# Optimization experiments

Measured on AMD Instinct MI355X. Metric: run time of the kernel, lower is better.

Reference implementation:

```python
import jax, jax.numpy as jnp
import numpy as np

N_NODES = 100000
N_EDGES = 1600000
D_IN = 128
HID = 256
N_CLASSES = 10
N_GRAPHS = 512


def setup_inputs() -> dict:
    key = jax.random.key(0)
    ks = jax.random.split(key, 12)
    x = jax.random.normal(ks[0], (N_NODES, D_IN), dtype=jnp.float32)
    edge_index = jax.random.randint(ks[1], (2, N_EDGES), 0, N_NODES, dtype=jnp.int32)
    batch = jnp.sort(jax.random.randint(ks[2], (N_NODES,), 0, N_GRAPHS, dtype=jnp.int32))
    s = 0.05
    return {
        "x": x,
        "edge_index": edge_index,
        "batch": batch,
        "W1": jax.random.normal(ks[3], (D_IN, HID), dtype=jnp.float32) * s,
        "b1": jnp.zeros((HID,), dtype=jnp.float32),
        "W2": jax.random.normal(ks[4], (HID, HID), dtype=jnp.float32) * s,
        "b2": jnp.zeros((HID,), dtype=jnp.float32),
        "fc1_w": jax.random.normal(ks[5], (HID, HID // 2), dtype=jnp.float32) * s,
        "fc1_b": jnp.zeros((HID // 2,), dtype=jnp.float32),
        "fc2_w": jax.random.normal(ks[6], (HID // 2, N_CLASSES), dtype=jnp.float32) * s,
        "fc2_b": jnp.zeros((N_CLASSES,), dtype=jnp.float32),
    }


def gcn_conv(x, src, dst, W, b, num_nodes):
    # PyG GCNConv: h = x @ W, add self-loops, sym-normalized scatter-add, + bias
    h = x @ W  # [N, out]
    loop = jnp.arange(num_nodes, dtype=src.dtype)
    s = jnp.concatenate([src, loop])
    d = jnp.concatenate([dst, loop])
    ones = jnp.ones(s.shape[0], dtype=h.dtype)
    deg = jax.ops.segment_sum(ones, d, num_segments=num_nodes)  # includes self-loops
    dinv = jax.lax.rsqrt(jnp.maximum(deg, 1.0))
    norm = dinv[s] * dinv[d]  # [E+N]
    msgs = h[s] * norm[:, None]  # gather + scale
    out = jax.ops.segment_sum(msgs, d, num_segments=num_nodes)  # scatter-add
    return out + b


def global_mean_pool(x, batch, num_graphs):
    sums = jax.ops.segment_sum(x, batch, num_segments=num_graphs)
    cnt = jax.ops.segment_sum(jnp.ones(x.shape[0], x.dtype), batch, num_segments=num_graphs)
    return sums / jnp.maximum(cnt, 1.0)[:, None]


def reference(x, edge_index, batch, W1, b1, W2, b2, fc1_w, fc1_b, fc2_w, fc2_b):
    src, dst = edge_index[0], edge_index[1]
    h = jax.nn.relu(gcn_conv(x, src, dst, W1, b1, N_NODES))
    h = jax.nn.relu(gcn_conv(h, src, dst, W2, b2, N_NODES))
    g = global_mean_pool(h, batch, N_GRAPHS)  # [G, HID]
    # dropout is identity in eval mode
    g = jax.nn.relu(g @ fc1_w + fc1_b)
    return g @ fc2_w + fc2_b  # [G, num_classes]
```

## Files before the change

kernel.cpp:

```cpp
#include <hip/hip_runtime.h>
#include <hip/hip_bf16.h>
#include <hip/hip_fp16.h>
#include <cstddef>

#define N_NODES 100000
#define N_EDGES 1600000
#define D_IN 128
#define HID 256
#define N_CLASSES 10
#define N_GRAPHS 512
#define CAP 64

typedef __attribute__((ext_vector_type(8))) short short8v;
typedef __attribute__((ext_vector_type(4))) float f32x4;
typedef _Float16 h2v __attribute__((ext_vector_type(2)));
typedef _Float16 h4v __attribute__((ext_vector_type(4)));
typedef _Float16 h8v __attribute__((ext_vector_type(8)));

__device__ __forceinline__ ushort f2bf(float x) {
    __hip_bfloat16 b = __float2bfloat16(x);
    return *reinterpret_cast<ushort*>(&b);
}
__device__ __forceinline__ float bf2f(ushort u) {
    __hip_bfloat16 b = *reinterpret_cast<__hip_bfloat16*>(&u);
    return __bfloat162float(b);
}

__global__ void zero_int_kernel(int* p, int n) {
    int i = blockIdx.x * blockDim.x + threadIdx.x;
    if (i < n) p[i] = 0;
}

__global__ void fill_bins_kernel(const int* __restrict__ src, const int* __restrict__ dst,
                                 int* __restrict__ cnt, int* __restrict__ bins) {
    int t = blockIdx.x * blockDim.x + threadIdx.x;
    int base = t * 4;
    if (base + 4 <= N_EDGES) {
        int4 d4 = *reinterpret_cast<const int4*>(dst + base);
        int4 s4 = *reinterpret_cast<const int4*>(src + base);
        int k0 = atomicAdd(&cnt[d4.x], 1);
        int k1 = atomicAdd(&cnt[d4.y], 1);
        int k2 = atomicAdd(&cnt[d4.z], 1);
        int k3 = atomicAdd(&cnt[d4.w], 1);
        if (k0 < CAP) __builtin_nontemporal_store(s4.x, &bins[(size_t)d4.x * CAP + k0]);
        if (k1 < CAP) __builtin_nontemporal_store(s4.y, &bins[(size_t)d4.y * CAP + k1]);
        if (k2 < CAP) __builtin_nontemporal_store(s4.z, &bins[(size_t)d4.z * CAP + k2]);
        if (k3 < CAP) __builtin_nontemporal_store(s4.w, &bins[(size_t)d4.w * CAP + k3]);
    } else {
        for (int e = base; e < N_EDGES; ++e) {
            int d = dst[e];
            int k = atomicAdd(&cnt[d], 1);
            if (k < CAP) __builtin_nontemporal_store(src[e], &bins[(size_t)d * CAP + k]);
        }
    }
}

__global__ void dinv_kernel(const int* __restrict__ cnt, float* __restrict__ dinv, int n) {
    int i = blockIdx.x * blockDim.x + threadIdx.x;
    if (i < n) dinv[i] = rsqrtf((float)(1 + cnt[i]));
}

__global__ void wsplit_kernel(const float* __restrict__ W, ushort* __restrict__ Wh,
                              ushort* __restrict__ Wl, int K, int M) {
    int idx = blockIdx.x * blockDim.x + threadIdx.x;
    if (idx >= M * K) return;
    int m = idx / K, k = idx - m * K;
    float v = W[(size_t)k * M + m];
    ushort h = f2bf(v);
    Wh[idx] = h;
    Wl[idx] = f2bf(v - bf2f(h));
}

__global__ void xscale_kernel(const float* __restrict__ x, const float* __restrict__ dinv,
                              _Float16* __restrict__ xh) {
    int idx = blockIdx.x * blockDim.x + threadIdx.x;
    if (idx >= N_NODES * D_IN / 8) return;
    int node = idx >> 4;
    float s = dinv[node];
    const float4 a = *reinterpret_cast<const float4*>(x + (size_t)idx * 8);
    const float4 b = *reinterpret_cast<const float4*>(x + (size_t)idx * 8 + 4);
    h8v o;
    o[0] = (_Float16)(a.x * s); o[1] = (_Float16)(a.y * s);
    o[2] = (_Float16)(a.z * s); o[3] = (_Float16)(a.w * s);
    o[4] = (_Float16)(b.x * s); o[5] = (_Float16)(b.y * s);
    o[6] = (_Float16)(b.z * s); o[7] = (_Float16)(b.w * s);
    *reinterpret_cast<h8v*>(xh + (size_t)idx * 8) = o;
}

#define GPAD 40
__global__ __launch_bounds__(256) void gemm_bf16x2_kernel(
    const ushort* __restrict__ Ah, const ushort* __restrict__ Al,
    const ushort* __restrict__ Bh, const ushort* __restrict__ Bl,
    _Float16* __restrict__ C, const float* __restrict__ bias,
    const float* __restrict__ rowscale, int N, int K, int M) {
    __shared__ ushort AhL[128 * GPAD];
    __shared__ ushort AlL[128 * GPAD];
    __shared__ ushort BhL[128 * GPAD];
    __shared__ ushort BlL[128 * GPAD];

    int tid = threadIdx.x;
    int lane = tid & 63, w = tid >> 6;
    int wr = w >> 1, wc = w & 1;
    int rowBase = blockIdx.y * 128;
    int colBase = blockIdx.x * 128;

    f32x4 acc[4][4];
#pragma unroll
    for (int m = 0; m < 4; ++m)
#pragma unroll
        for (int n = 0; n < 4; ++n) acc[m][n] = (f32x4)(0.0f);

    const uint4 zero4 = make_uint4(0, 0, 0, 0);

    for (int k0 = 0; k0 < K; k0 += 32) {
#pragma unroll
        for (int c = 0; c < 2; ++c) {
            int idx = c * 256 + tid;
            int r = idx >> 2, q = idx & 3;
            int lds = r * GPAD + q * 8;
            size_t ga = (size_t)(rowBase + r) * K + k0 + q * 8;
            uint4 va = zero4, vl = zero4;
            if (rowBase + r < N) {
                va = *reinterpret_cast<const uint4*>(Ah + ga);
                vl = *reinterpret_cast<const uint4*>(Al + ga);
            }
            *reinterpret_cast<uint4*>(&AhL[lds]) = va;
            *reinterpret_cast<uint4*>(&AlL[lds]) = vl;
            size_t gb = (size_t)(colBase + r) * K + k0 + q * 8;
            *reinterpret_cast<uint4*>(&BhL[lds]) = *reinterpret_cast<const uint4*>(Bh + gb);
            *reinterpret_cast<uint4*>(&BlL[lds]) = *reinterpret_cast<const uint4*>(Bl + gb);
        }
        __syncthreads();

        short8v afh[4], afl[4], bfh[4], bfl[4];
        int kg = (lane >> 4) * 8;
#pragma unroll
        for (int m = 0; m < 4; ++m) {
            int r = wr * 64 + m * 16 + (lane & 15);
            afh[m] = *reinterpret_cast<const short8v*>(&AhL[r * GPAD + kg]);
            afl[m] = *reinterpret_cast<const short8v*>(&AlL[r * GPAD + kg]);
        }
#pragma unroll
        for (int n = 0; n < 4; ++n) {
            int r = wc * 64 + n * 16 + (lane & 15);
            bfh[n] = *reinterpret_cast<const short8v*>(&BhL[r * GPAD + kg]);
            bfl[n] = *reinterpret_cast<const short8v*>(&BlL[r * GPAD + kg]);
        }
#pragma unroll
        for (int m = 0; m < 4; ++m)
#pragma unroll
            for (int n = 0; n < 4; ++n) {
                acc[m][n] = __builtin_amdgcn_mfma_f32_16x16x32_bf16(afh[m], bfh[n], acc[m][n], 0, 0, 0);
                acc[m][n] = __builtin_amdgcn_mfma_f32_16x16x32_bf16(afh[m], bfl[n], acc[m][n], 0, 0, 0);
                acc[m][n] = __builtin_amdgcn_mfma_f32_16x16x32_bf16(afl[m], bfh[n], acc[m][n], 0, 0, 0);
            }
        __syncthreads();
    }

    float bv[4];
#pragma unroll
    for (int n = 0; n < 4; ++n)
        bv[n] = bias[colBase + wc * 64 + n * 16 + (lane & 15)];

#pragma unroll
    for (int m = 0; m < 4; ++m) {
#pragma unroll
        for (int reg = 0; reg < 4; ++reg) {
            int row = rowBase + wr * 64 + m * 16 + (lane >> 4) * 4 + reg;
            if (row < N) {
                float sc = rowscale ? rowscale[row] : 1.0f;
#pragma unroll
                for (int n = 0; n < 4; ++n) {
                    int col = colBase + wc * 64 + n * 16 + (lane & 15);
                    C[(size_t)row * M + col] = (_Float16)(fmaxf(acc[m][n][reg] + bv[n], 0.0f) * sc);
                }
            }
        }
    }
}

__global__ __launch_bounds__(256) void gather_h_kernel(
    const _Float16* __restrict__ hf, const int* __restrict__ bins,
    const int* __restrict__ cnt, const float* __restrict__ dinv,
    ushort* __restrict__ aggH, ushort* __restrict__ aggL) {
    int node = blockIdx.x * 4 + (threadIdx.x >> 6);
    if (node >= N_NODES) return;
    int lane = threadIdx.x & 63;
    const size_t dimOff = (size_t)lane * 4;
    const size_t binBase = (size_t)node * CAP;

    h4v hv = *reinterpret_cast<const h4v*>(hf + (size_t)node * HID + dimOff);
    float4 a[4];
    a[0] = make_float4((float)hv[0], (float)hv[1], (float)hv[2], (float)hv[3]);
    a[1] = make_float4(0.f, 0.f, 0.f, 0.f);
    a[2] = make_float4(0.f, 0.f, 0.f, 0.f);
    a[3] = make_float4(0.f, 0.f, 0.f, 0.f);

    int end = min(cnt[node], CAP);
    int e = 0;
    for (; e + 12 <= end; e += 12) {
        int ss[12];
#pragma unroll
        for (int k = 0; k < 12; ++k) ss[k] = bins[binBase + e + k];
        h4v vv[12];
#pragma unroll
        for (int k = 0; k < 12; ++k)
            vv[k] = *reinterpret_cast<const h4v*>(hf + (size_t)ss[k] * HID + dimOff);
#pragma unroll
        for (int k = 0; k < 12; ++k) {
            a[k & 3].x += (float)vv[k][0];
            a[k & 3].y += (float)vv[k][1];
            a[k & 3].z += (float)vv[k][2];
            a[k & 3].w += (float)vv[k][3];
        }
    }
    for (; e < end; ++e) {
        int s = bins[binBase + e];
        h4v v = *reinterpret_cast<const h4v*>(hf + (size_t)s * HID + dimOff);
        a[0].x += (float)v[0]; a[0].y += (float)v[1];
        a[0].z += (float)v[2]; a[0].w += (float)v[3];
    }
    float dn = dinv[node];
    float4 acc = make_float4(((a[0].x + a[1].x) + (a[2].x + a[3].x)) * dn,
                             ((a[0].y + a[1].y) + (a[2].y + a[3].y)) * dn,
                             ((a[0].z + a[1].z) + (a[2].z + a[3].z)) * dn,
                             ((a[0].w + a[1].w) + (a[2].w + a[3].w)) * dn);
    ushort4 hh, ll;
    hh.x = f2bf(acc.x); ll.x = f2bf(acc.x - bf2f(hh.x));
    hh.y = f2bf(acc.y); ll.y = f2bf(acc.y - bf2f(hh.y));
    hh.z = f2bf(acc.z); ll.z = f2bf(acc.z - bf2f(hh.z));
    hh.w = f2bf(acc.w); ll.w = f2bf(acc.w - bf2f(hh.w));
    *reinterpret_cast<ushort4*>(aggH + (size_t)node * HID + dimOff) = hh;
    *reinterpret_cast<ushort4*>(aggL + (size_t)node * HID + dimOff) = ll;
}

__global__ __launch_bounds__(256) void gather_x_kernel(
    const _Float16* __restrict__ xh, const int* __restrict__ bins,
    const int* __restrict__ cnt, const float* __restrict__ dinv,
    ushort* __restrict__ aggH, ushort* __restrict__ aggL) {
    int node = blockIdx.x * 4 + (threadIdx.x >> 6);
    if (node >= N_NODES) return;
    int lane = threadIdx.x & 63;
    const size_t dimOff = (size_t)lane * 2;
    const size_t binBase = (size_t)node * CAP;

    h2v hv = *reinterpret_cast<const h2v*>(xh + (size_t)node * D_IN + dimOff);
    float2 a[4];
    a[0] = make_float2((float)hv[0], (float)hv[1]);
    a[1] = make_float2(0.f, 0.f);
    a[2] = make_float2(0.f, 0.f);
    a[3] = make_float2(0.f, 0.f);

    int end = min(cnt[node], CAP);
    int e = 0;
    for (; e + 12 <= end; e += 12) {
        int ss[12];
#pragma unroll
        for (int k = 0; k < 12; ++k) ss[k] = bins[binBase + e + k];
        h2v vv[12];
#pragma unroll
        for (int k = 0; k < 12; ++k)
            vv[k] = *reinterpret_cast<const h2v*>(xh + (size_t)ss[k] * D_IN + dimOff);
#pragma unroll
        for (int k = 0; k < 12; ++k) {
            a[k & 3].x += (float)vv[k][0];
            a[k & 3].y += (float)vv[k][1];
        }
    }
    for (; e < end; ++e) {
        int s = bins[binBase + e];
        h2v v = *reinterpret_cast<const h2v*>(xh + (size_t)s * D_IN + dimOff);
        a[0].x += (float)v[0]; a[0].y += (float)v[1];
    }
    float dn = dinv[node];
    float2 acc = make_float2(((a[0].x + a[1].x) + (a[2].x + a[3].x)) * dn,
                             ((a[0].y + a[1].y) + (a[2].y + a[3].y)) * dn);
    ushort2 hh, ll;
    hh.x = f2bf(acc.x); ll.x = f2bf(acc.x - bf2f(hh.x));
    hh.y = f2bf(acc.y); ll.y = f2bf(acc.y - bf2f(hh.y));
    *reinterpret_cast<ushort2*>(aggH + (size_t)node * D_IN + dimOff) = hh;
    *reinterpret_cast<ushort2*>(aggL + (size_t)node * D_IN + dimOff) = ll;
}

__global__ __launch_bounds__(256) void pool_head_kernel(
    const _Float16* __restrict__ h, const int* __restrict__ batch,
    const float* __restrict__ fc1_w, const float* __restrict__ fc1_b,
    const float* __restrict__ fc2_w, const float* __restrict__ fc2_b,
    float* __restrict__ out) {
    __shared__ int sRange[2];
    __shared__ float gbuf[HID];
    __shared__ float hbuf[HID / 2];
    int g = blockIdx.x;
    int tid = threadIdx.x;

    if (tid < 2) {
        int target = g + tid;
        int lo = 0, hi = N_NODES;
        while (lo < hi) {
            int mid = (lo + hi) >> 1;
            if (batch[mid] < target) lo = mid + 1; else hi = mid;
        }
        sRange[tid] = lo;
    }
    __syncthreads();
    int beg = sRange[0], end = sRange[1];

    float acc = 0.f;
    int n = beg;
    for (; n + 4 <= end; n += 4) {
        float v0 = (float)h[(size_t)(n + 0) * HID + tid];
        float v1 = (float)h[(size_t)(n + 1) * HID + tid];
        float v2 = (float)h[(size_t)(n + 2) * HID + tid];
        float v3 = (float)h[(size_t)(n + 3) * HID + tid];
        acc += (v0 + v1) + (v2 + v3);
    }
    for (; n < end; ++n) acc += (float)h[(size_t)n * HID + tid];
    float c = fmaxf((float)(end - beg), 1.0f);
    gbuf[tid] = acc / c;
    __syncthreads();

    if (tid < HID / 2) {
        float a = fc1_b[tid];
        for (int k = 0; k < HID; ++k) a += gbuf[k] * fc1_w[(size_t)k * (HID / 2) + tid];
        hbuf[tid] = fmaxf(a, 0.0f);
    }
    __syncthreads();
    if (tid < N_CLASSES) {
        float a = fc2_b[tid];
        for (int k = 0; k < HID / 2; ++k) a += hbuf[k] * fc2_w[(size_t)k * N_CLASSES + tid];
        out[(size_t)g * N_CLASSES + tid] = a;
    }
}

extern "C" void kernel_launch(void* const* d_in, const int* in_sizes, int n_in,
                              void* d_out, int out_size, void* d_ws, size_t ws_size,
                              hipStream_t stream) {
    const float* x     = (const float*)d_in[0];
    const int* eidx    = (const int*)d_in[1];
    const int* batch   = (const int*)d_in[2];
    const float* W1    = (const float*)d_in[3];
    const float* b1    = (const float*)d_in[4];
    const float* W2    = (const float*)d_in[5];
    const float* b2    = (const float*)d_in[6];
    const float* fc1_w = (const float*)d_in[7];
    const float* fc1_b = (const float*)d_in[8];
    const float* fc2_w = (const float*)d_in[9];
    const float* fc2_b = (const float*)d_in[10];
    float* out = (float*)d_out;

    const int* src = eidx;
    const int* dst = eidx + N_EDGES;

    _Float16* h16  = (_Float16*)d_ws;
    _Float16* xh   = h16;
    ushort* R2     = (ushort*)(h16 + (size_t)N_NODES * HID);
    ushort* aggXh  = R2;
    ushort* aggXl  = R2 + (size_t)N_NODES * D_IN;
    ushort* aggHh  = R2;
    ushort* aggHl  = R2 + (size_t)N_NODES * HID;
    int* bins      = (int*)(R2 + (size_t)2 * N_NODES * HID);
    ushort* Wt1h   = (ushort*)(bins + (size_t)N_NODES * CAP);
    ushort* Wt1l   = Wt1h + HID * D_IN;
    ushort* Wt2h   = Wt1l + HID * D_IN;
    ushort* Wt2l   = Wt2h + HID * HID;
    float* dinv    = (float*)(Wt2l + HID * HID);
    int* cnt       = (int*)(dinv + N_NODES);

    const int nB = (N_NODES + 255) / 256;

    zero_int_kernel<<<nB, 256, 0, stream>>>(cnt, N_NODES);
    fill_bins_kernel<<<(N_EDGES / 4 + 255) / 256, 256, 0, stream>>>(src, dst, cnt, bins);
    dinv_kernel<<<nB, 256, 0, stream>>>(cnt, dinv, N_NODES);

    wsplit_kernel<<<(HID * D_IN + 255) / 256, 256, 0, stream>>>(W1, Wt1h, Wt1l, D_IN, HID);
    wsplit_kernel<<<(HID * HID + 255) / 256, 256, 0, stream>>>(W2, Wt2h, Wt2l, HID, HID);
    xscale_kernel<<<(N_NODES * D_IN / 8 + 255) / 256, 256, 0, stream>>>(x, dinv, xh);

    const int gatherBlocks = (N_NODES + 3) / 4;
    dim3 gemmGrid(HID / 128, (N_NODES + 127) / 128);

    gather_x_kernel<<<gatherBlocks, 256, 0, stream>>>(xh, bins, cnt, dinv, aggXh, aggXl);
    gemm_bf16x2_kernel<<<gemmGrid, 256, 0, stream>>>(aggXh, aggXl, Wt1h, Wt1l, h16, b1, dinv,
                                                     N_NODES, D_IN, HID);

    gather_h_kernel<<<gatherBlocks, 256, 0, stream>>>(h16, bins, cnt, dinv, aggHh, aggHl);
    gemm_bf16x2_kernel<<<gemmGrid, 256, 0, stream>>>(aggHh, aggHl, Wt2h, Wt2l, h16, b2, nullptr,
                                                     N_NODES, HID, HID);

    pool_head_kernel<<<N_GRAPHS, 256, 0, stream>>>(h16, batch, fc1_w, fc1_b, fc2_w, fc2_b, out);
}
```

Before: 621.0 us.

## Load neighbor bins once per wave and broadcast indices via shuffles

In both gather kernels each lane now loads one bin entry in a single coalesced read, and neighbor indices are broadcast with __shfl, replacing the scalar-uniform loads from the bins array. The unroll depth drops from 12 to 8. fill_bins goes back to one edge per thread with plain stores instead of vectorized int4 loads and nontemporal stores, and the zero kernel becomes hipMemsetAsync. The shuffles add cross-lane ops, the smaller unroll lowers memory-level parallelism, and the simpler fill kernel may change the cost of the scatter.

New measurement: 549.0 us. -11.6%, faster.

```diff
diff --git a/kernel.cpp b/kernel.cpp
--- a/kernel.cpp
+++ b/kernel.cpp
@@ -26,32 +26,13 @@
     return __bfloat162float(b);
 }
 
-__global__ void zero_int_kernel(int* p, int n) {
-    int i = blockIdx.x * blockDim.x + threadIdx.x;
-    if (i < n) p[i] = 0;
-}
-
 __global__ void fill_bins_kernel(const int* __restrict__ src, const int* __restrict__ dst,
-                                 int* __restrict__ cnt, int* __restrict__ bins) {
-    int t = blockIdx.x * blockDim.x + threadIdx.x;
-    int base = t * 4;
-    if (base + 4 <= N_EDGES) {
-        int4 d4 = *reinterpret_cast<const int4*>(dst + base);
-        int4 s4 = *reinterpret_cast<const int4*>(src + base);
-        int k0 = atomicAdd(&cnt[d4.x], 1);
-        int k1 = atomicAdd(&cnt[d4.y], 1);
-        int k2 = atomicAdd(&cnt[d4.z], 1);
-        int k3 = atomicAdd(&cnt[d4.w], 1);
-        if (k0 < CAP) __builtin_nontemporal_store(s4.x, &bins[(size_t)d4.x * CAP + k0]);
-        if (k1 < CAP) __builtin_nontemporal_store(s4.y, &bins[(size_t)d4.y * CAP + k1]);
-        if (k2 < CAP) __builtin_nontemporal_store(s4.z, &bins[(size_t)d4.z * CAP + k2]);
-        if (k3 < CAP) __builtin_nontemporal_store(s4.w, &bins[(size_t)d4.w * CAP + k3]);
-    } else {
-        for (int e = base; e < N_EDGES; ++e) {
-            int d = dst[e];
-            int k = atomicAdd(&cnt[d], 1);
-            if (k < CAP) __builtin_nontemporal_store(src[e], &bins[(size_t)d * CAP + k]);
-        }
+                                 int* __restrict__ cnt, int* __restrict__ bins, int nE) {
+    int e = blockIdx.x * blockDim.x + threadIdx.x;
+    if (e < nE) {
+        int d = dst[e];
+        int k = atomicAdd(&cnt[d], 1);
+        if (k < CAP) bins[(size_t)d * CAP + k] = src[e];
     }
 }
 
@@ -187,7 +168,9 @@
     if (node >= N_NODES) return;
     int lane = threadIdx.x & 63;
     const size_t dimOff = (size_t)lane * 4;
-    const size_t binBase = (size_t)node * CAP;
+
+    int myBin = bins[(size_t)node * CAP + lane];
+    int end = min(cnt[node], CAP);
 
     h4v hv = *reinterpret_cast<const h4v*>(hf + (size_t)node * HID + dimOff);
     float4 a[4];
@@ -196,18 +179,17 @@
     a[2] = make_float4(0.f, 0.f, 0.f, 0.f);
     a[3] = make_float4(0.f, 0.f, 0.f, 0.f);
 
-    int end = min(cnt[node], CAP);
     int e = 0;
-    for (; e + 12 <= end; e += 12) {
-        int ss[12];
-#pragma unroll
-        for (int k = 0; k < 12; ++k) ss[k] = bins[binBase + e + k];
-        h4v vv[12];
-#pragma unroll
-        for (int k = 0; k < 12; ++k)
+    for (; e + 8 <= end; e += 8) {
+        int ss[8];
+#pragma unroll
+        for (int k = 0; k < 8; ++k) ss[k] = __shfl(myBin, e + k);
+        h4v vv[8];
+#pragma unroll
+        for (int k = 0; k < 8; ++k)
             vv[k] = *reinterpret_cast<const h4v*>(hf + (size_t)ss[k] * HID + dimOff);
 #pragma unroll
-        for (int k = 0; k < 12; ++k) {
+        for (int k = 0; k < 8; ++k) {
             a[k & 3].x += (float)vv[k][0];
             a[k & 3].y += (float)vv[k][1];
             a[k & 3].z += (float)vv[k][2];
@@ -215,7 +197,7 @@
         }
     }
     for (; e < end; ++e) {
-        int s = bins[binBase + e];
+        int s = __shfl(myBin, e);
         h4v v = *reinterpret_cast<const h4v*>(hf + (size_t)s * HID + dimOff);
         a[0].x += (float)v[0]; a[0].y += (float)v[1];
         a[0].z += (float)v[2]; a[0].w += (float)v[3];
@@ -242,7 +224,9 @@
     if (node >= N_NODES) return;
     int lane = threadIdx.x & 63;
     const size_t dimOff = (size_t)lane * 2;
-    const size_t binBase = (size_t)node * CAP;
+
+    int myBin = bins[(size_t)node * CAP + lane];
+    int end = min(cnt[node], CAP);
 
     h2v hv = *reinterpret_cast<const h2v*>(xh + (size_t)node * D_IN + dimOff);
     float2 a[4];
@@ -251,24 +235,23 @@
     a[2] = make_float2(0.f, 0.f);
     a[3] = make_float2(0.f, 0.f);
 
-    int end = min(cnt[node], CAP);
     int e = 0;
-    for (; e + 12 <= end; e += 12) {
-        int ss[12];
-#pragma unroll
-        for (int k = 0; k < 12; ++k) ss[k] = bins[binBase + e + k];
-        h2v vv[12];
-#pragma unroll
-        for (int k = 0; k < 12; ++k)
+    for (; e + 8 <= end; e += 8) {
+        int ss[8];
+#pragma unroll
+        for (int k = 0; k < 8; ++k) ss[k] = __shfl(myBin, e + k);
+        h2v vv[8];
+#pragma unroll
+        for (int k = 0; k < 8; ++k)
             vv[k] = *reinterpret_cast<const h2v*>(xh + (size_t)ss[k] * D_IN + dimOff);
 #pragma unroll
-        for (int k = 0; k < 12; ++k) {
+        for (int k = 0; k < 8; ++k) {
             a[k & 3].x += (float)vv[k][0];
             a[k & 3].y += (float)vv[k][1];
         }
     }
     for (; e < end; ++e) {
-        int s = bins[binBase + e];
+        int s = __shfl(myBin, e);
         h2v v = *reinterpret_cast<const h2v*>(xh + (size_t)s * D_IN + dimOff);
         a[0].x += (float)v[0]; a[0].y += (float)v[1];
     }
@@ -367,9 +350,10 @@
     int* cnt       = (int*)(dinv + N_NODES);
 
     const int nB = (N_NODES + 255) / 256;
-
-    zero_int_kernel<<<nB, 256, 0, stream>>>(cnt, N_NODES);
-    fill_bins_kernel<<<(N_EDGES / 4 + 255) / 256, 256, 0, stream>>>(src, dst, cnt, bins);
+    const int eB = (N_EDGES + 255) / 256;
+
+    hipMemsetAsync(cnt, 0, (size_t)N_NODES * sizeof(int), stream);
+    fill_bins_kernel<<<eB, 256, 0, stream>>>(src, dst, cnt, bins, N_EDGES);
     dinv_kernel<<<nB, 256, 0, stream>>>(cnt, dinv, N_NODES);
 
     wsplit_kernel<<<(HID * D_IN + 255) / 256, 256, 0, stream>>>(W1, Wt1h, Wt1l, D_IN, HID);
```
